# Optimization experiments

Hardware: AMD Instinct MI355X
Metric: run time of the kernel (lower is better)

Reference implementation:

```python
import jax, jax.numpy as jnp
import numpy as np

B, T, S, D = 4, 4, 128, 256  # batch, turns, seq_len, hidden_size
H = D  # GRU units == hidden_size


def setup_inputs() -> dict:
    key = jax.random.key(0)
    ks = jax.random.split(key, 8)
    sc = lambda *sh: float(np.sqrt(2.0 / sum(sh[:2]))) if len(sh) > 1 else 0.05
    return {
        "features": jax.random.normal(ks[0], (B, T, S, D), jnp.float32),
        "w1": jax.random.normal(ks[1], (D, D), jnp.float32) * sc(D, D),
        "w2": jax.random.normal(ks[2], (D, D), jnp.float32) * sc(D, D),
        "bias": jax.random.normal(ks[3], (D,), jnp.float32) * 0.05,
        "v3": jax.random.normal(ks[4], (D,), jnp.float32) * 0.05,
        "gru_kernel": jax.random.normal(ks[5], (2 * D, 3 * H), jnp.float32) * sc(2 * D, 3 * H),
        "gru_rec_kernel": jax.random.normal(ks[6], (H, 3 * H), jnp.float32) * sc(H, 3 * H),
        "gru_bias": jax.random.normal(ks[7], (2, 3 * H), jnp.float32) * 0.05,
    }


def _gru(x, kernel, rec_kernel, bias):
    # x: [N, S, 2D]; Keras GRU (reset_after=True, tanh/sigmoid), h0 = 0.
    b_in, b_rec = bias[0], bias[1]
    xp = x @ kernel + b_in               # [N, S, 3H] input projections
    xp_t = jnp.swapaxes(xp, 0, 1)        # [S, N, 3H]
    h0 = jnp.zeros((x.shape[0], H), x.dtype)

    def step(h, xt):
        rp = h @ rec_kernel + b_rec      # [N, 3H]
        xz, xr, xh = jnp.split(xt, 3, axis=-1)
        rz, rr, rh = jnp.split(rp, 3, axis=-1)
        z = jax.nn.sigmoid(xz + rz)
        r = jax.nn.sigmoid(xr + rr)
        hh = jnp.tanh(xh + r * rh)
        h_new = z * h + (1.0 - z) * hh
        return h_new, h_new

    _, ys = jax.lax.scan(step, h0, xp_t)  # ys: [S, N, H]
    return jnp.swapaxes(ys, 0, 1)         # [N, S, H]


def reference(features, w1, w2, bias, v3, gru_kernel, gru_rec_kernel, gru_bias):
    b, t, s, d = features.shape
    x = features.reshape(b * t, s, d)     # fold turns into batch (same per-utterance math)
    left = jnp.einsum('bsd,dt->bst', x, w1)
    right = jnp.einsum('bsd,dt->bst', x, w2)
    # additive (Bahdanau) scores: [N, s, s, d] intermediate
    temp = jnp.tanh(left[:, :, None, :] + right[:, None, :, :] + bias)
    score = jax.nn.softmax(jnp.einsum('bmnd,d->bmn', temp, v3), axis=-1)
    c = jnp.einsum('bmn,bnd->bmd', score, x)
    p = _gru(jnp.concatenate([x, c], axis=-1), gru_kernel, gru_rec_kernel, gru_bias)
    return p.reshape(b, t, s, H)
```

## Files before the change

### kernel.cpp

```cpp
#include <hip/hip_runtime.h>
#include <hip/hip_bf16.h>

typedef __attribute__((ext_vector_type(8))) short short8;
typedef __attribute__((ext_vector_type(4))) float floatx4;

#define NSEQ 16
#define SEQ 128
#define DIM 256
#define HID 256
#define K3H 768
#define K2D 512
#define LOG2E 1.442695041f
#define LOG2E2 2.885390082f
#define WS_STRIDE 772

__device__ __forceinline__ float frcp(float x) { return __builtin_amdgcn_rcpf(x); }
__device__ __forceinline__ unsigned short bf16bits(float v) {
    unsigned u = __builtin_bit_cast(unsigned, v);
    unsigned r = (u + 0x7FFFu + ((u >> 16) & 1u)) >> 16;
    return (unsigned short)r;
}
__device__ __forceinline__ void load_lds16(const float* gsrc, float* ldsbase) {
    __builtin_amdgcn_global_load_lds(
        (const __attribute__((address_space(1))) void*)gsrc,
        (__attribute__((address_space(3))) void*)ldsbase, 16, 0, 0);
}

__global__ __launch_bounds__(256) void k1_leftright(
        const float* __restrict__ x, const float* __restrict__ w1,
        const float* __restrict__ w2, float* __restrict__ left,
        float* __restrict__ right) {
    __shared__ __align__(16) float xs[8][DIM];
    const int tid = threadIdx.x;
    const int r0 = blockIdx.x * 8;
    #pragma unroll
    for (int i = 0; i < 8; ++i) xs[i][tid] = x[(r0 + i) * DIM + tid];
    __syncthreads();
    float accL[8], accR[8];
    #pragma unroll
    for (int i = 0; i < 8; ++i) { accL[i] = 0.f; accR[i] = 0.f; }
    #pragma unroll 4
    for (int d = 0; d < DIM; ++d) {
        float wa = w1[d * DIM + tid];
        float wb = w2[d * DIM + tid];
        #pragma unroll
        for (int i = 0; i < 8; ++i) {
            float xv = xs[i][d];
            accL[i] = fmaf(xv, wa, accL[i]);
            accR[i] = fmaf(xv, wb, accR[i]);
        }
    }
    #pragma unroll
    for (int i = 0; i < 8; ++i) {
        left[(r0 + i) * DIM + tid]  = accL[i] * LOG2E2;
        right[(r0 + i) * DIM + tid] = accR[i] * LOG2E2;
    }
}

__global__ __launch_bounds__(256) void k2_attn(
        const float* __restrict__ x, const float* __restrict__ left,
        const float* __restrict__ right, const float* __restrict__ bias,
        const float* __restrict__ v3, float* __restrict__ cout) {
    __shared__ __align__(16) float lm[4][DIM];
    __shared__ __align__(16) float v3s[DIM];
    __shared__ __align__(16) float P[4][SEQ];
    const int tid = threadIdx.x;
    const int b  = blockIdx.x >> 5;
    const int m0 = (blockIdx.x & 31) * 4;

    v3s[tid] = v3[tid];
    #pragma unroll
    for (int i = 0; i < 4; ++i)
        lm[i][tid] = left[(size_t)(b * SEQ + m0 + i) * DIM + tid] + bias[tid] * LOG2E2;
    __syncthreads();

    const int mi = tid >> 6;
    const int nl = tid & 63;
    float s0 = 0.f, s1 = 0.f;
    const float4* lv4 = reinterpret_cast<const float4*>(lm[mi]);
    const float4* vv4 = reinterpret_cast<const float4*>(v3s);
    const float4* r0v = reinterpret_cast<const float4*>(right + (size_t)(b * SEQ + nl) * DIM);
    const float4* r1v = reinterpret_cast<const float4*>(right + (size_t)(b * SEQ + nl + 64) * DIM);
    #pragma unroll 2
    for (int d4 = 0; d4 < DIM / 4; ++d4) {
        float4 lv = lv4[d4];
        float4 vv = vv4[d4];
        float4 ra = r0v[d4];
        float4 rb = r1v[d4];
        float a0 = 1.f - 2.f * frcp(1.f + __builtin_amdgcn_exp2f(lv.x + ra.x));
        float a1 = 1.f - 2.f * frcp(1.f + __builtin_amdgcn_exp2f(lv.y + ra.y));
        float a2 = 1.f - 2.f * frcp(1.f + __builtin_amdgcn_exp2f(lv.z + ra.z));
        float a3 = 1.f - 2.f * frcp(1.f + __builtin_amdgcn_exp2f(lv.w + ra.w));
        s0 = fmaf(a0, vv.x, s0); s0 = fmaf(a1, vv.y, s0);
        s0 = fmaf(a2, vv.z, s0); s0 = fmaf(a3, vv.w, s0);
        float b0 = 1.f - 2.f * frcp(1.f + __builtin_amdgcn_exp2f(lv.x + rb.x));
        float b1 = 1.f - 2.f * frcp(1.f + __builtin_amdgcn_exp2f(lv.y + rb.y));
        float b2 = 1.f - 2.f * frcp(1.f + __builtin_amdgcn_exp2f(lv.z + rb.z));
        float b3 = 1.f - 2.f * frcp(1.f + __builtin_amdgcn_exp2f(lv.w + rb.w));
        s1 = fmaf(b0, vv.x, s1); s1 = fmaf(b1, vv.y, s1);
        s1 = fmaf(b2, vv.z, s1); s1 = fmaf(b3, vv.w, s1);
    }
    float mx = fmaxf(s0, s1);
    #pragma unroll
    for (int off = 32; off >= 1; off >>= 1) mx = fmaxf(mx, __shfl_xor(mx, off, 64));
    float e0 = __expf(s0 - mx), e1 = __expf(s1 - mx);
    float sm = e0 + e1;
    #pragma unroll
    for (int off = 32; off >= 1; off >>= 1) sm += __shfl_xor(sm, off, 64);
    float inv = frcp(sm);
    P[mi][nl]      = e0 * inv;
    P[mi][nl + 64] = e1 * inv;
    __syncthreads();

    float acc[4] = {0.f, 0.f, 0.f, 0.f};
    const float* xb = x + (size_t)b * SEQ * DIM;
    for (int nc = 0; nc < SEQ / 4; ++nc) {
        float xv0 = xb[(nc * 4 + 0) * DIM + tid];
        float xv1 = xb[(nc * 4 + 1) * DIM + tid];
        float xv2 = xb[(nc * 4 + 2) * DIM + tid];
        float xv3 = xb[(nc * 4 + 3) * DIM + tid];
        #pragma unroll
        for (int i = 0; i < 4; ++i) {
            float4 pv = *reinterpret_cast<const float4*>(&P[i][nc * 4]);
            acc[i] = fmaf(pv.x, xv0, acc[i]);
            acc[i] = fmaf(pv.y, xv1, acc[i]);
            acc[i] = fmaf(pv.z, xv2, acc[i]);
            acc[i] = fmaf(pv.w, xv3, acc[i]);
        }
    }
    #pragma unroll
    for (int i = 0; i < 4; ++i)
        cout[(size_t)(b * SEQ + m0 + i) * DIM + tid] = acc[i];
}

__global__ __launch_bounds__(512) void k3_mfma(
        const float* __restrict__ x, const float* __restrict__ c,
        const float* __restrict__ gk, const float* __restrict__ gbias,
        float* __restrict__ xp) {
    __shared__ __align__(16) unsigned short As[64][72];
    __shared__ __align__(16) unsigned short Bs[192][72];
    const int tid  = threadIdx.x;
    const int lane = tid & 63;
    const int w    = tid >> 6;
    const int l15  = lane & 15;
    const int g4   = lane >> 4;
    const int wm   = w >> 2;
    const int wn   = w & 3;
    const int m0   = (blockIdx.x & 31) * 64;
    const int n0   = (blockIdx.x >> 5) * 192;

    floatx4 Cf[2][3];
    #pragma unroll
    for (int i = 0; i < 2; ++i)
        #pragma unroll
        for (int j = 0; j < 3; ++j) Cf[i][j] = (floatx4){0.f, 0.f, 0.f, 0.f};

    for (int ch = 0; ch < 8; ++ch) {
        const int kbase = ch * 64;
        #pragma unroll
        for (int q = 0; q < 2; ++q) {
            int fi = q * 512 + tid;
            int row = fi >> 4, kq = (fi & 15) << 2;
            int kg = kbase + kq;
            const float* src = (kg < 256) ? &x[(size_t)(m0 + row) * DIM + kg]
                                          : &c[(size_t)(m0 + row) * DIM + (kg - 256)];
            float4 v = *reinterpret_cast<const float4*>(src);
            unsigned short* dst = &As[row][kq];
            dst[0] = bf16bits(v.x); dst[1] = bf16bits(v.y);
            dst[2] = bf16bits(v.z); dst[3] = bf16bits(v.w);
        }
        #pragma unroll
        for (int q = 0; q < 6; ++q) {
            int fi = q * 512 + tid;
            int krow = fi / 48, nq = (fi % 48) << 2;
            float4 v = *reinterpret_cast<const float4*>(
                &gk[(size_t)(kbase + krow) * K3H + n0 + nq]);
            Bs[nq + 0][krow] = bf16bits(v.x);
            Bs[nq + 1][krow] = bf16bits(v.y);
            Bs[nq + 2][krow] = bf16bits(v.z);
            Bs[nq + 3][krow] = bf16bits(v.w);
        }
        __syncthreads();
        #pragma unroll
        for (int kk = 0; kk < 2; ++kk) {
            short8 af[2], bf[3];
            #pragma unroll
            for (int i = 0; i < 2; ++i)
                af[i] = *reinterpret_cast<const short8*>(&As[wm * 32 + i * 16 + l15][kk * 32 + g4 * 8]);
            #pragma unroll
            for (int j = 0; j < 3; ++j)
                bf[j] = *reinterpret_cast<const short8*>(&Bs[wn * 48 + j * 16 + l15][kk * 32 + g4 * 8]);
            #pragma unroll
            for (int i = 0; i < 2; ++i)
                #pragma unroll
                for (int j = 0; j < 3; ++j)
                    Cf[i][j] = __builtin_amdgcn_mfma_f32_16x16x32_bf16(af[i], bf[j], Cf[i][j], 0, 0, 0);
        }
        __syncthreads();
    }

    #pragma unroll
    for (int j = 0; j < 3; ++j) {
        const int nbase = n0 + wn * 48 + j * 16;
        const int col = nbase + l15;
        const float sc = (nbase >= 512) ? LOG2E2 : LOG2E;
        const float bv = ((col < 512) ? (gbias[col] + gbias[K3H + col]) : gbias[col]) * sc;
        #pragma unroll
        for (int i = 0; i < 2; ++i) {
            const int rbase = m0 + wm * 32 + i * 16 + g4 * 4;
            #pragma unroll
            for (int r = 0; r < 4; ++r)
                xp[(size_t)(rbase + r) * K3H + col] = fmaf(Cf[i][j][r], sc, bv);
        }
    }
}

__global__ __launch_bounds__(512) void k4_gru(
        const float* __restrict__ rec, const float* __restrict__ gbias,
        const float* __restrict__ xp, float* __restrict__ out) {
    __shared__ __align__(16) float ws[16 * WS_STRIDE];
    __shared__ __align__(16) float xq0[K3H], xq1[K3H], xq2[K3H];
    __shared__ __align__(16) unsigned short hbf[2][HID];
    const int tid  = threadIdx.x;
    const int lane = tid & 63;
    const int wv   = tid >> 6;
    const int seq  = blockIdx.x;
    const int l15  = lane & 15;
    const int g4   = lane >> 4;

    short8 Bf[6][8];
    #pragma unroll
    for (int part = 0; part < 16; ++part) {
        #pragma unroll
        for (int q = 0; q < 6; ++q) {
            int fi = q * 512 + tid;
            int row = fi / 192, c4 = fi % 192;
            reinterpret_cast<float4*>(ws)[row * (WS_STRIDE / 4) + c4] =
                reinterpret_cast<const float4*>(rec + part * 16 * K3H)[fi];
        }
        __syncthreads();
        const int kc = part >> 1, half = part & 1;
        #pragma unroll
        for (int u = 0; u < 6; ++u) {
            const float sc = (u >= 4) ? LOG2E2 : LOG2E;
            const int col = (u >> 1) * 256 + (u & 1) * 16 + wv * 32 + l15;
            #pragma unroll
            for (int j = 0; j < 8; ++j) {
                int r = g4 * 8 + j;
                if ((r >> 4) == half)
                    Bf[u][kc][j] = (short)bf16bits(ws[(r & 15) * WS_STRIDE + col] * sc);
            }
        }
        __syncthreads();
    }

    const int dd = wv * 32 + (lane & 31);
    const float brh_l = gbias[K3H + 512 + dd] * LOG2E2;
    const int tsel = (lane >> 4) & 1;

    const float* xps = xp + (size_t)seq * SEQ * K3H;
    float* outs = out + (size_t)seq * SEQ * HID;

    float h = 0.f;
    if (tid < HID) hbf[0][tid] = 0;

    if (wv < 3) {
        load_lds16(xps + wv * 256 + (lane << 2),       xq0 + wv * 256);
        load_lds16(xps + K3H + wv * 256 + (lane << 2), xq1 + wv * 256);
    }
    asm volatile("s_waitcnt vmcnt(0)" ::: "memory");
    __syncthreads();

    float* p0 = xq0;
    float* p1 = xq1;
    float* p2 = xq2;

    #define K4_STEP(s_, CB, NB)                                                         \
    {                                                                                   \
        const int sp = ((s_) + 2 < SEQ) ? (s_) + 2 : SEQ - 1;                           \
        if (wv < 3)                                                                     \
            load_lds16(xps + (size_t)sp * K3H + wv * 256 + (lane << 2), p2 + wv * 256); \
        short8 av[8];                                                                   \
        _Pragma("unroll")                                                               \
        for (int kc = 0; kc < 8; ++kc)                                                  \
            av[kc] = *reinterpret_cast<const short8*>(&hbf[CB][kc * 32 + g4 * 8]);      \
        const float xz = p0[dd];                                                        \
        const float xr = p0[256 + dd];                                                  \
        const float xh = p0[512 + dd];                                                  \
        floatx4 C[6];                                                                   \
        _Pragma("unroll")                                                               \
        for (int u = 0; u < 6; ++u) C[u] = (floatx4){0.f, 0.f, 0.f, 0.f};               \
        _Pragma("unroll")                                                               \
        for (int kc = 0; kc < 8; ++kc) {                                                \
            _Pragma("unroll")                                                           \
            for (int u = 0; u < 6; ++u)                                                 \
                C[u] = __builtin_amdgcn_mfma_f32_16x16x32_bf16(av[kc], Bf[u][kc],       \
                                                               C[u], 0, 0, 0);         \
        }                                                                               \
        if (lane < 32) {                                                                \
            float rz = tsel ? C[1][0] : C[0][0];                                        \
            float rr = tsel ? C[3][0] : C[2][0];                                        \
            float rh = tsel ? C[5][0] : C[4][0];                                        \
            float z  = frcp(1.f + __builtin_amdgcn_exp2f(-(rz + xz)));                  \
            float r  = frcp(1.f + __builtin_amdgcn_exp2f(-(rr + xr)));                  \
            float th = fmaf(r, rh + brh_l, xh);                                         \
            float hh = 1.f - 2.f * frcp(1.f + __builtin_amdgcn_exp2f(th));              \
            h = hh + z * (h - hh);                                                      \
            hbf[NB][dd] = bf16bits(h);                                                  \
            outs[(s_) * HID + dd] = h;                                                  \
        }                                                                               \
        asm volatile("s_waitcnt vmcnt(3) lgkmcnt(0)\n\ts_barrier" ::: "memory");        \
        float* tmp_ = p0; p0 = p1; p1 = p2; p2 = tmp_;                                  \
    }

    for (int s = 0; s < SEQ; s += 2) {
        K4_STEP(s,     0, 1)
        K4_STEP(s + 1, 1, 0)
    }
    #undef K4_STEP
}

extern "C" void kernel_launch(void* const* d_in, const int* in_sizes, int n_in,
                              void* d_out, int out_size, void* d_ws, size_t ws_size,
                              hipStream_t stream) {
    const float* feat = (const float*)d_in[0];
    const float* w1   = (const float*)d_in[1];
    const float* w2   = (const float*)d_in[2];
    const float* bias = (const float*)d_in[3];
    const float* v3   = (const float*)d_in[4];
    const float* gk   = (const float*)d_in[5];
    const float* grk  = (const float*)d_in[6];
    const float* gb   = (const float*)d_in[7];
    float* out = (float*)d_out;

    char* wsb = (char*)d_ws;
    float* left  = (float*)(wsb);
    float* right = (float*)(wsb + (size_t)2 * 1024 * 1024);
    float* cbuf  = (float*)(wsb + (size_t)4 * 1024 * 1024);
    float* xp    = (float*)(wsb + (size_t)6 * 1024 * 1024);

    k1_leftright<<<2048 / 8, 256, 0, stream>>>(feat, w1, w2, left, right);
    k2_attn<<<NSEQ * 32, 256, 0, stream>>>(feat, left, right, bias, v3, cbuf);
    k3_mfma<<<128, 512, 0, stream>>>(feat, cbuf, gk, gb, xp);
    k4_gru<<<NSEQ, 512, 0, stream>>>(grk, gb, xp, out);
}
```

Before: 238.0 us.

## Fuse all four stages into one persistent kernel with atomic-flag dataflow

Merges the four kernels (left/right projection, attention, input projection GEMM, GRU recurrence) into a single launch. Block ranges are assigned to stages, and global atomic counters act as dependency flags. The GRU blocks preload their recurrent weights into registers while upstream stages are still running, and start the recurrence once the first half of the input projections is ready. This is meant to remove launch gaps and overlap the serial GRU setup with producer work. The cost is spin-waiting on flags, a memset, and reliance on all 528 blocks being co-resident to avoid deadlock.

```diff
diff --git a/kernel.cpp b/kernel.cpp
--- a/kernel.cpp
+++ b/kernel.cpp
@@ -26,298 +26,339 @@
         (__attribute__((address_space(3))) void*)ldsbase, 16, 0, 0);
 }
 
-__global__ __launch_bounds__(256) void k1_leftright(
+__global__ __launch_bounds__(512) void k_fused(
         const float* __restrict__ x, const float* __restrict__ w1,
-        const float* __restrict__ w2, float* __restrict__ left,
-        float* __restrict__ right) {
-    __shared__ __align__(16) float xs[8][DIM];
+        const float* __restrict__ w2, const float* __restrict__ bias,
+        const float* __restrict__ v3, const float* __restrict__ gk,
+        const float* __restrict__ rec, const float* __restrict__ gb,
+        float* __restrict__ left, float* __restrict__ right,
+        float* __restrict__ cbuf, float* __restrict__ xp,
+        float* __restrict__ out, unsigned* __restrict__ flags) {
+    __shared__ __align__(16) char smem[59648];
+    unsigned* f1 = flags;
+    unsigned* f2 = flags + 16;
+    unsigned* f3 = flags + 48;
+    const int bid = blockIdx.x;
     const int tid = threadIdx.x;
-    const int r0 = blockIdx.x * 8;
-    #pragma unroll
-    for (int i = 0; i < 8; ++i) xs[i][tid] = x[(r0 + i) * DIM + tid];
-    __syncthreads();
-    float accL[8], accR[8];
-    #pragma unroll
-    for (int i = 0; i < 8; ++i) { accL[i] = 0.f; accR[i] = 0.f; }
-    #pragma unroll 4
-    for (int d = 0; d < DIM; ++d) {
-        float wa = w1[d * DIM + tid];
-        float wb = w2[d * DIM + tid];
+
+    if (bid < 16) {
+        float* ws = (float*)smem;
+        float* xqa = (float*)(smem + 49408);
+        float* xqb = (float*)(smem + 52480);
+        float* xqc = (float*)(smem + 55552);
+        unsigned short (*hbf)[HID] = (unsigned short(*)[HID])(smem + 58624);
+        const int lane = tid & 63;
+        const int wv   = tid >> 6;
+        const int seq  = bid;
+        const int l15  = lane & 15;
+        const int g4   = lane >> 4;
+
+        short8 Bf[6][8];
+        #pragma unroll
+        for (int part = 0; part < 16; ++part) {
+            #pragma unroll
+            for (int q = 0; q < 6; ++q) {
+                int fi = q * 512 + tid;
+                int row = fi / 192, c4 = fi % 192;
+                reinterpret_cast<float4*>(ws)[row * (WS_STRIDE / 4) + c4] =
+                    reinterpret_cast<const float4*>(rec + part * 16 * K3H)[fi];
+            }
+            __syncthreads();
+            const int kc = part >> 1, half = part & 1;
+            #pragma unroll
+            for (int u = 0; u < 6; ++u) {
+                const float sc = (u >= 4) ? LOG2E2 : LOG2E;
+                const int col = (u >> 1) * 256 + (u & 1) * 16 + wv * 32 + l15;
+                #pragma unroll
+                for (int j = 0; j < 8; ++j) {
+                    int r = g4 * 8 + j;
+                    if ((r >> 4) == half)
+                        Bf[u][kc][j] = (short)bf16bits(ws[(r & 15) * WS_STRIDE + col] * sc);
+                }
+            }
+            __syncthreads();
+        }
+
+        const int dd = wv * 32 + (lane & 31);
+        const float brh_l = gb[K3H + 512 + dd] * LOG2E2;
+        const int tsel = (lane >> 4) & 1;
+        const float* xps = xp + (size_t)seq * SEQ * K3H;
+        float* outs = out + (size_t)seq * SEQ * HID;
+        float h = 0.f;
+        if (tid < HID) hbf[0][tid] = 0;
+
+        if (tid == 0) { while (atomicAdd(&f3[seq * 2], 0u) < 4u) __builtin_amdgcn_s_sleep(2); }
+        __syncthreads();
+        __threadfence();
+
+        if (wv < 3) {
+            load_lds16(xps + wv * 256 + (lane << 2),       xqa + wv * 256);
+            load_lds16(xps + K3H + wv * 256 + (lane << 2), xqb + wv * 256);
+        }
+        asm volatile("s_waitcnt vmcnt(0)" ::: "memory");
+        __syncthreads();
+
+        float* p0 = xqa;
+        float* p1 = xqb;
+        float* p2 = xqc;
+
+        #define K4_STEP(s_, CB, NB)                                                         \
+        {                                                                                   \
+            const int sp = ((s_) + 2 < SEQ) ? (s_) + 2 : SEQ - 1;                           \
+            if (wv < 3)                                                                     \
+                load_lds16(xps + (size_t)sp * K3H + wv * 256 + (lane << 2), p2 + wv * 256); \
+            short8 av[8];                                                                   \
+            _Pragma("unroll")                                                               \
+            for (int kc = 0; kc < 8; ++kc)                                                  \
+                av[kc] = *reinterpret_cast<const short8*>(&hbf[CB][kc * 32 + g4 * 8]);      \
+            const float xz = p0[dd];                                                        \
+            const float xr = p0[256 + dd];                                                  \
+            const float xh = p0[512 + dd];                                                  \
+            floatx4 C[6];                                                                   \
+            _Pragma("unroll")                                                               \
+            for (int u = 0; u < 6; ++u) C[u] = (floatx4){0.f, 0.f, 0.f, 0.f};               \
+            _Pragma("unroll")                                                               \
+            for (int kc = 0; kc < 8; ++kc) {                                                \
+                _Pragma("unroll")                                                           \
+                for (int u = 0; u < 6; ++u)                                                 \
+                    C[u] = __builtin_amdgcn_mfma_f32_16x16x32_bf16(av[kc], Bf[u][kc],       \
+                                                                   C[u], 0, 0, 0);         \
+            }                                                                               \
+            if (lane < 32) {                                                                \
+                float rz = tsel ? C[1][0] : C[0][0];                                        \
+                float rr = tsel ? C[3][0] : C[2][0];                                        \
+                float rh = tsel ? C[5][0] : C[4][0];                                        \
+                float z  = frcp(1.f + __builtin_amdgcn_exp2f(-(rz + xz)));                  \
+                float r  = frcp(1.f + __builtin_amdgcn_exp2f(-(rr + xr)));                  \
+                float th = fmaf(r, rh + brh_l, xh);                                         \
+                float hh = 1.f - 2.f * frcp(1.f + __builtin_amdgcn_exp2f(th));              \
+                h = hh + z * (h - hh);                                                      \
+                hbf[NB][dd] = bf16bits(h);                                                  \
+                outs[(s_) * HID + dd] = h;                                                  \
+            }                                                                               \
+            asm volatile("s_waitcnt vmcnt(3) lgkmcnt(0)\n\ts_barrier" ::: "memory");        \
+            float* tmp_ = p0; p0 = p1; p1 = p2; p2 = tmp_;                                  \
+        }
+
+        for (int s = 0; s < 62; s += 2) {
+            K4_STEP(s,     0, 1)
+            K4_STEP(s + 1, 1, 0)
+        }
+        if (tid == 0) { while (atomicAdd(&f3[seq * 2 + 1], 0u) < 4u) __builtin_amdgcn_s_sleep(2); }
+        __syncthreads();
+        __threadfence();
+        for (int s = 62; s < SEQ; s += 2) {
+            K4_STEP(s,     0, 1)
+            K4_STEP(s + 1, 1, 0)
+        }
+        #undef K4_STEP
+
+    } else if (bid < 144) {
+        const int kb = bid - 16;
+        const int r0 = kb * 16;
+        float (*xs)[DIM] = (float(*)[DIM])smem;
+        const int col = tid & 255, hf = tid >> 8;
+        #pragma unroll
+        for (int i = 0; i < 8; ++i)
+            xs[hf * 8 + i][col] = x[(size_t)(r0 + hf * 8 + i) * DIM + col];
+        __syncthreads();
+        float accL[8], accR[8];
+        #pragma unroll
+        for (int i = 0; i < 8; ++i) { accL[i] = 0.f; accR[i] = 0.f; }
+        #pragma unroll 4
+        for (int d = 0; d < DIM; ++d) {
+            float wa = w1[d * DIM + col];
+            float wb = w2[d * DIM + col];
+            #pragma unroll
+            for (int i = 0; i < 8; ++i) {
+                float xv = xs[hf * 8 + i][d];
+                accL[i] = fmaf(xv, wa, accL[i]);
+                accR[i] = fmaf(xv, wb, accR[i]);
+            }
+        }
         #pragma unroll
         for (int i = 0; i < 8; ++i) {
-            float xv = xs[i][d];
-            accL[i] = fmaf(xv, wa, accL[i]);
-            accR[i] = fmaf(xv, wb, accR[i]);
-        }
+            left[(size_t)(r0 + hf * 8 + i) * DIM + col]  = accL[i] * LOG2E2;
+            right[(size_t)(r0 + hf * 8 + i) * DIM + col] = accR[i] * LOG2E2;
+        }
+        __threadfence();
+        __syncthreads();
+        if (tid == 0) atomicAdd(&f1[kb >> 3], 1u);
+
+    } else if (bid < 400) {
+        const int kb = bid - 144;
+        const int b  = kb >> 4;
+        const int m0 = (kb & 15) * 8;
+        float (*lm)[DIM] = (float(*)[DIM])smem;
+        float* v3s = (float*)(smem + 8192);
+        float (*P)[SEQ] = (float(*)[SEQ])(smem + 9216);
+
+        if (tid == 0) { while (atomicAdd(&f1[b], 0u) < 8u) __builtin_amdgcn_s_sleep(2); }
+        __syncthreads();
+        __threadfence();
+
+        {
+            const int col = tid & 255, hf = tid >> 8;
+            #pragma unroll
+            for (int i = 0; i < 4; ++i)
+                lm[hf * 4 + i][col] =
+                    left[(size_t)(b * SEQ + m0 + hf * 4 + i) * DIM + col] + bias[col] * LOG2E2;
+            if (tid < 256) v3s[tid] = v3[tid];
+        }
+        __syncthreads();
+
+        const int w  = tid >> 6;
+        const int nl = tid & 63;
+        float s0 = 0.f, s1 = 0.f;
+        const float4* lv4 = reinterpret_cast<const float4*>(lm[w]);
+        const float4* vv4 = reinterpret_cast<const float4*>(v3s);
+        const float4* r0v = reinterpret_cast<const float4*>(right + (size_t)(b * SEQ + nl) * DIM);
+        const float4* r1v = reinterpret_cast<const float4*>(right + (size_t)(b * SEQ + nl + 64) * DIM);
+        #pragma unroll 2
+        for (int d4 = 0; d4 < DIM / 4; ++d4) {
+            float4 lv = lv4[d4];
+            float4 vv = vv4[d4];
+            float4 ra = r0v[d4];
+            float4 rb = r1v[d4];
+            float a0 = 1.f - 2.f * frcp(1.f + __builtin_amdgcn_exp2f(lv.x + ra.x));
+            float a1 = 1.f - 2.f * frcp(1.f + __builtin_amdgcn_exp2f(lv.y + ra.y));
+            float a2 = 1.f - 2.f * frcp(1.f + __builtin_amdgcn_exp2f(lv.z + ra.z));
+            float a3 = 1.f - 2.f * frcp(1.f + __builtin_amdgcn_exp2f(lv.w + ra.w));
+            s0 = fmaf(a0, vv.x, s0); s0 = fmaf(a1, vv.y, s0);
+            s0 = fmaf(a2, vv.z, s0); s0 = fmaf(a3, vv.w, s0);
+            float b0 = 1.f - 2.f * frcp(1.f + __builtin_amdgcn_exp2f(lv.x + rb.x));
+            float b1 = 1.f - 2.f * frcp(1.f + __builtin_amdgcn_exp2f(lv.y + rb.y));
+            float b2 = 1.f - 2.f * frcp(1.f + __builtin_amdgcn_exp2f(lv.z + rb.z));
+            float b3 = 1.f - 2.f * frcp(1.f + __builtin_amdgcn_exp2f(lv.w + rb.w));
+            s1 = fmaf(b0, vv.x, s1); s1 = fmaf(b1, vv.y, s1);
+            s1 = fmaf(b2, vv.z, s1); s1 = fmaf(b3, vv.w, s1);
+        }
+        float mx = fmaxf(s0, s1);
+        #pragma unroll
+        for (int off = 32; off >= 1; off >>= 1) mx = fmaxf(mx, __shfl_xor(mx, off, 64));
+        float e0 = __expf(s0 - mx), e1 = __expf(s1 - mx);
+        float sm = e0 + e1;
+        #pragma unroll
+        for (int off = 32; off >= 1; off >>= 1) sm += __shfl_xor(sm, off, 64);
+        float inv = frcp(sm);
+        P[w][nl]      = e0 * inv;
+        P[w][nl + 64] = e1 * inv;
+        __syncthreads();
+
+        const int d  = tid & 255;
+        const int rg = tid >> 8;
+        float acc[4] = {0.f, 0.f, 0.f, 0.f};
+        const float* xb = x + (size_t)b * SEQ * DIM;
+        for (int nc = 0; nc < SEQ / 4; ++nc) {
+            float xv0 = xb[(nc * 4 + 0) * DIM + d];
+            float xv1 = xb[(nc * 4 + 1) * DIM + d];
+            float xv2 = xb[(nc * 4 + 2) * DIM + d];
+            float xv3 = xb[(nc * 4 + 3) * DIM + d];
+            #pragma unroll
+            for (int i = 0; i < 4; ++i) {
+                float4 pv = *reinterpret_cast<const float4*>(&P[rg * 4 + i][nc * 4]);
+                acc[i] = fmaf(pv.x, xv0, acc[i]);
+                acc[i] = fmaf(pv.y, xv1, acc[i]);
+                acc[i] = fmaf(pv.z, xv2, acc[i]);
+                acc[i] = fmaf(pv.w, xv3, acc[i]);
+            }
+        }
+        #pragma unroll
+        for (int i = 0; i < 4; ++i)
+            cbuf[(size_t)(b * SEQ + m0 + rg * 4 + i) * DIM + d] = acc[i];
+        __threadfence();
+        __syncthreads();
+        if (tid == 0) atomicAdd(&f2[b * 2 + (m0 >> 6)], 1u);
+
+    } else {
+        const int kb = bid - 400;
+        unsigned short (*As)[72] = (unsigned short(*)[72])smem;
+        unsigned short (*Bs)[72] = (unsigned short(*)[72])(smem + 9216);
+        const int lane = tid & 63;
+        const int w    = tid >> 6;
+        const int l15  = lane & 15;
+        const int g4   = lane >> 4;
+        const int wm   = w >> 2;
+        const int wn   = w & 3;
+        const int mt   = kb & 31;
+        const int m0   = mt * 64;
+        const int n0   = (kb >> 5) * 192;
+
+        if (tid == 0) {
+            while (atomicAdd(&f2[(m0 >> 7) * 2 + ((m0 >> 6) & 1)], 0u) < 8u)
+                __builtin_amdgcn_s_sleep(2);
+        }
+        __syncthreads();
+        __threadfence();
+
+        floatx4 Cf[2][3];
+        #pragma unroll
+        for (int i = 0; i < 2; ++i)
+            #pragma unroll
+            for (int j = 0; j < 3; ++j) Cf[i][j] = (floatx4){0.f, 0.f, 0.f, 0.f};
+
+        for (int ch = 0; ch < 8; ++ch) {
+            const int kbase = ch * 64;
+            #pragma unroll
+            for (int q = 0; q < 2; ++q) {
+                int fi = q * 512 + tid;
+                int row = fi >> 4, kq = (fi & 15) << 2;
+                int kg = kbase + kq;
+                const float* src = (kg < 256) ? &x[(size_t)(m0 + row) * DIM + kg]
+                                              : &cbuf[(size_t)(m0 + row) * DIM + (kg - 256)];
+                float4 v = *reinterpret_cast<const float4*>(src);
+                unsigned short* dst = &As[row][kq];
+                dst[0] = bf16bits(v.x); dst[1] = bf16bits(v.y);
+                dst[2] = bf16bits(v.z); dst[3] = bf16bits(v.w);
+            }
+            #pragma unroll
+            for (int q = 0; q < 6; ++q) {
+                int fi = q * 512 + tid;
+                int krow = fi / 48, nq = (fi % 48) << 2;
+                float4 v = *reinterpret_cast<const float4*>(
+                    &gk[(size_t)(kbase + krow) * K3H + n0 + nq]);
+                Bs[nq + 0][krow] = bf16bits(v.x);
+                Bs[nq + 1][krow] = bf16bits(v.y);
+                Bs[nq + 2][krow] = bf16bits(v.z);
+                Bs[nq + 3][krow] = bf16bits(v.w);
+            }
+            __syncthreads();
+            #pragma unroll
+            for (int kk = 0; kk < 2; ++kk) {
+                short8 af[2], bf[3];
+                #pragma unroll
+                for (int i = 0; i < 2; ++i)
+                    af[i] = *reinterpret_cast<const short8*>(&As[wm * 32 + i * 16 + l15][kk * 32 + g4 * 8]);
+                #pragma unroll
+                for (int j = 0; j < 3; ++j)
+                    bf[j] = *reinterpret_cast<const short8*>(&Bs[wn * 48 + j * 16 + l15][kk * 32 + g4 * 8]);
+                #pragma unroll
+                for (int i = 0; i < 2; ++i)
+                    #pragma unroll
+                    for (int j = 0; j < 3; ++j)
+                        Cf[i][j] = __builtin_amdgcn_mfma_f32_16x16x32_bf16(af[i], bf[j], Cf[i][j], 0, 0, 0);
+            }
+            __syncthreads();
+        }
+
+        #pragma unroll
+        for (int j = 0; j < 3; ++j) {
+            const int nbase = n0 + wn * 48 + j * 16;
+            const int col = nbase + l15;
+            const float sc = (nbase >= 512) ? LOG2E2 : LOG2E;
+            const float bv = ((col < 512) ? (gb[col] + gb[K3H + col]) : gb[col]) * sc;
+            #pragma unroll
+            for (int i = 0; i < 2; ++i) {
+                const int rbase = m0 + wm * 32 + i * 16 + g4 * 4;
+                #pragma unroll
+                for (int r = 0; r < 4; ++r)
+                    xp[(size_t)(rbase + r) * K3H + col] = fmaf(Cf[i][j][r], sc, bv);
+            }
+        }
+        __threadfence();
+        __syncthreads();
+        if (tid == 0) atomicAdd(&f3[mt], 1u);
     }
-    #pragma unroll
-    for (int i = 0; i < 8; ++i) {
-        left[(r0 + i) * DIM + tid]  = accL[i] * LOG2E2;
-        right[(r0 + i) * DIM + tid] = accR[i] * LOG2E2;
-    }
-}
-
-__global__ __launch_bounds__(256) void k2_attn(
-        const float* __restrict__ x, const float* __restrict__ left,
-        const float* __restrict__ right, const float* __restrict__ bias,
-        const float* __restrict__ v3, float* __restrict__ cout) {
-    __shared__ __align__(16) float lm[4][DIM];
-    __shared__ __align__(16) float v3s[DIM];
-    __shared__ __align__(16) float P[4][SEQ];
-    const int tid = threadIdx.x;
-    const int b  = blockIdx.x >> 5;
-    const int m0 = (blockIdx.x & 31) * 4;
-
-    v3s[tid] = v3[tid];
-    #pragma unroll
-    for (int i = 0; i < 4; ++i)
-        lm[i][tid] = left[(size_t)(b * SEQ + m0 + i) * DIM + tid] + bias[tid] * LOG2E2;
-    __syncthreads();
-
-    const int mi = tid >> 6;
-    const int nl = tid & 63;
-    float s0 = 0.f, s1 = 0.f;
-    const float4* lv4 = reinterpret_cast<const float4*>(lm[mi]);
-    const float4* vv4 = reinterpret_cast<const float4*>(v3s);
-    const float4* r0v = reinterpret_cast<const float4*>(right + (size_t)(b * SEQ + nl) * DIM);
-    const float4* r1v = reinterpret_cast<const float4*>(right + (size_t)(b * SEQ + nl + 64) * DIM);
-    #pragma unroll 2
-    for (int d4 = 0; d4 < DIM / 4; ++d4) {
-        float4 lv = lv4[d4];
-        float4 vv = vv4[d4];
-        float4 ra = r0v[d4];
-        float4 rb = r1v[d4];
-        float a0 = 1.f - 2.f * frcp(1.f + __builtin_amdgcn_exp2f(lv.x + ra.x));
-        float a1 = 1.f - 2.f * frcp(1.f + __builtin_amdgcn_exp2f(lv.y + ra.y));
-        float a2 = 1.f - 2.f * frcp(1.f + __builtin_amdgcn_exp2f(lv.z + ra.z));
-        float a3 = 1.f - 2.f * frcp(1.f + __builtin_amdgcn_exp2f(lv.w + ra.w));
-        s0 = fmaf(a0, vv.x, s0); s0 = fmaf(a1, vv.y, s0);
-        s0 = fmaf(a2, vv.z, s0); s0 = fmaf(a3, vv.w, s0);
-        float b0 = 1.f - 2.f * frcp(1.f + __builtin_amdgcn_exp2f(lv.x + rb.x));
-        float b1 = 1.f - 2.f * frcp(1.f + __builtin_amdgcn_exp2f(lv.y + rb.y));
-        float b2 = 1.f - 2.f * frcp(1.f + __builtin_amdgcn_exp2f(lv.z + rb.z));
-        float b3 = 1.f - 2.f * frcp(1.f + __builtin_amdgcn_exp2f(lv.w + rb.w));
-        s1 = fmaf(b0, vv.x, s1); s1 = fmaf(b1, vv.y, s1);
-        s1 = fmaf(b2, vv.z, s1); s1 = fmaf(b3, vv.w, s1);
-    }
-    float mx = fmaxf(s0, s1);
-    #pragma unroll
-    for (int off = 32; off >= 1; off >>= 1) mx = fmaxf(mx, __shfl_xor(mx, off, 64));
-    float e0 = __expf(s0 - mx), e1 = __expf(s1 - mx);
-    float sm = e0 + e1;
-    #pragma unroll
-    for (int off = 32; off >= 1; off >>= 1) sm += __shfl_xor(sm, off, 64);
-    float inv = frcp(sm);
-    P[mi][nl]      = e0 * inv;
-    P[mi][nl + 64] = e1 * inv;
-    __syncthreads();
-
-    float acc[4] = {0.f, 0.f, 0.f, 0.f};
-    const float* xb = x + (size_t)b * SEQ * DIM;
-    for (int nc = 0; nc < SEQ / 4; ++nc) {
-        float xv0 = xb[(nc * 4 + 0) * DIM + tid];
-        float xv1 = xb[(nc * 4 + 1) * DIM + tid];
-        float xv2 = xb[(nc * 4 + 2) * DIM + tid];
-        float xv3 = xb[(nc * 4 + 3) * DIM + tid];
-        #pragma unroll
-        for (int i = 0; i < 4; ++i) {
-            float4 pv = *reinterpret_cast<const float4*>(&P[i][nc * 4]);
-            acc[i] = fmaf(pv.x, xv0, acc[i]);
-            acc[i] = fmaf(pv.y, xv1, acc[i]);
-            acc[i] = fmaf(pv.z, xv2, acc[i]);
-            acc[i] = fmaf(pv.w, xv3, acc[i]);
-        }
-    }
-    #pragma unroll
-    for (int i = 0; i < 4; ++i)
-        cout[(size_t)(b * SEQ + m0 + i) * DIM + tid] = acc[i];
-}
-
-__global__ __launch_bounds__(512) void k3_mfma(
-        const float* __restrict__ x, const float* __restrict__ c,
-        const float* __restrict__ gk, const float* __restrict__ gbias,
-        float* __restrict__ xp) {
-    __shared__ __align__(16) unsigned short As[64][72];
-    __shared__ __align__(16) unsigned short Bs[192][72];
-    const int tid  = threadIdx.x;
-    const int lane = tid & 63;
-    const int w    = tid >> 6;
-    const int l15  = lane & 15;
-    const int g4   = lane >> 4;
-    const int wm   = w >> 2;
-    const int wn   = w & 3;
-    const int m0   = (blockIdx.x & 31) * 64;
-    const int n0   = (blockIdx.x >> 5) * 192;
-
-    floatx4 Cf[2][3];
-    #pragma unroll
-    for (int i = 0; i < 2; ++i)
-        #pragma unroll
-        for (int j = 0; j < 3; ++j) Cf[i][j] = (floatx4){0.f, 0.f, 0.f, 0.f};
-
-    for (int ch = 0; ch < 8; ++ch) {
-        const int kbase = ch * 64;
-        #pragma unroll
-        for (int q = 0; q < 2; ++q) {
-            int fi = q * 512 + tid;
-            int row = fi >> 4, kq = (fi & 15) << 2;
-            int kg = kbase + kq;
-            const float* src = (kg < 256) ? &x[(size_t)(m0 + row) * DIM + kg]
-                                          : &c[(size_t)(m0 + row) * DIM + (kg - 256)];
-            float4 v = *reinterpret_cast<const float4*>(src);
-            unsigned short* dst = &As[row][kq];
-            dst[0] = bf16bits(v.x); dst[1] = bf16bits(v.y);
-            dst[2] = bf16bits(v.z); dst[3] = bf16bits(v.w);
-        }
-        #pragma unroll
-        for (int q = 0; q < 6; ++q) {
-            int fi = q * 512 + tid;
-            int krow = fi / 48, nq = (fi % 48) << 2;
-            float4 v = *reinterpret_cast<const float4*>(
-                &gk[(size_t)(kbase + krow) * K3H + n0 + nq]);
-            Bs[nq + 0][krow] = bf16bits(v.x);
-            Bs[nq + 1][krow] = bf16bits(v.y);
-            Bs[nq + 2][krow] = bf16bits(v.z);
-            Bs[nq + 3][krow] = bf16bits(v.w);
-        }
-        __syncthreads();
-        #pragma unroll
-        for (int kk = 0; kk < 2; ++kk) {
-            short8 af[2], bf[3];
-            #pragma unroll
-            for (int i = 0; i < 2; ++i)
-                af[i] = *reinterpret_cast<const short8*>(&As[wm * 32 + i * 16 + l15][kk * 32 + g4 * 8]);
-            #pragma unroll
-            for (int j = 0; j < 3; ++j)
-                bf[j] = *reinterpret_cast<const short8*>(&Bs[wn * 48 + j * 16 + l15][kk * 32 + g4 * 8]);
-            #pragma unroll
-            for (int i = 0; i < 2; ++i)
-                #pragma unroll
-                for (int j = 0; j < 3; ++j)
-                    Cf[i][j] = __builtin_amdgcn_mfma_f32_16x16x32_bf16(af[i], bf[j], Cf[i][j], 0, 0, 0);
-        }
-        __syncthreads();
-    }
-
-    #pragma unroll
-    for (int j = 0; j < 3; ++j) {
-        const int nbase = n0 + wn * 48 + j * 16;
-        const int col = nbase + l15;
-        const float sc = (nbase >= 512) ? LOG2E2 : LOG2E;
-        const float bv = ((col < 512) ? (gbias[col] + gbias[K3H + col]) : gbias[col]) * sc;
-        #pragma unroll
-        for (int i = 0; i < 2; ++i) {
-            const int rbase = m0 + wm * 32 + i * 16 + g4 * 4;
-            #pragma unroll
-            for (int r = 0; r < 4; ++r)
-                xp[(size_t)(rbase + r) * K3H + col] = fmaf(Cf[i][j][r], sc, bv);
-        }
-    }
-}
-
-__global__ __launch_bounds__(512) void k4_gru(
-        const float* __restrict__ rec, const float* __restrict__ gbias,
-        const float* __restrict__ xp, float* __restrict__ out) {
-    __shared__ __align__(16) float ws[16 * WS_STRIDE];
-    __shared__ __align__(16) float xq0[K3H], xq1[K3H], xq2[K3H];
-    __shared__ __align__(16) unsigned short hbf[2][HID];
-    const int tid  = threadIdx.x;
-    const int lane = tid & 63;
-    const int wv   = tid >> 6;
-    const int seq  = blockIdx.x;
-    const int l15  = lane & 15;
-    const int g4   = lane >> 4;
-
-    short8 Bf[6][8];
-    #pragma unroll
-    for (int part = 0; part < 16; ++part) {
-        #pragma unroll
-        for (int q = 0; q < 6; ++q) {
-            int fi = q * 512 + tid;
-            int row = fi / 192, c4 = fi % 192;
-            reinterpret_cast<float4*>(ws)[row * (WS_STRIDE / 4) + c4] =
-                reinterpret_cast<const float4*>(rec + part * 16 * K3H)[fi];
-        }
-        __syncthreads();
-        const int kc = part >> 1, half = part & 1;
-        #pragma unroll
-        for (int u = 0; u < 6; ++u) {
-            const float sc = (u >= 4) ? LOG2E2 : LOG2E;
-            const int col = (u >> 1) * 256 + (u & 1) * 16 + wv * 32 + l15;
-            #pragma unroll
-            for (int j = 0; j < 8; ++j) {
-                int r = g4 * 8 + j;
-                if ((r >> 4) == half)
-                    Bf[u][kc][j] = (short)bf16bits(ws[(r & 15) * WS_STRIDE + col] * sc);
-            }
-        }
-        __syncthreads();
-    }
-
-    const int dd = wv * 32 + (lane & 31);
-    const float brh_l = gbias[K3H + 512 + dd] * LOG2E2;
-    const int tsel = (lane >> 4) & 1;
-
-    const float* xps = xp + (size_t)seq * SEQ * K3H;
-    float* outs = out + (size_t)seq * SEQ * HID;
-
-    float h = 0.f;
-    if (tid < HID) hbf[0][tid] = 0;
-
-    if (wv < 3) {
-        load_lds16(xps + wv * 256 + (lane << 2),       xq0 + wv * 256);
-        load_lds16(xps + K3H + wv * 256 + (lane << 2), xq1 + wv * 256);
-    }
-    asm volatile("s_waitcnt vmcnt(0)" ::: "memory");
-    __syncthreads();
-
-    float* p0 = xq0;
-    float* p1 = xq1;
-    float* p2 = xq2;
-
-    #define K4_STEP(s_, CB, NB)                                                         \
-    {                                                                                   \
-        const int sp = ((s_) + 2 < SEQ) ? (s_) + 2 : SEQ - 1;                           \
-        if (wv < 3)                                                                     \
-            load_lds16(xps + (size_t)sp * K3H + wv * 256 + (lane << 2), p2 + wv * 256); \
-        short8 av[8];                                                                   \
-        _Pragma("unroll")                                                               \
-        for (int kc = 0; kc < 8; ++kc)                                                  \
-            av[kc] = *reinterpret_cast<const short8*>(&hbf[CB][kc * 32 + g4 * 8]);      \
-        const float xz = p0[dd];                                                        \
-        const float xr = p0[256 + dd];                                                  \
-        const float xh = p0[512 + dd];                                                  \
-        floatx4 C[6];                                                                   \
-        _Pragma("unroll")                                                               \
-        for (int u = 0; u < 6; ++u) C[u] = (floatx4){0.f, 0.f, 0.f, 0.f};               \
-        _Pragma("unroll")                                                               \
-        for (int kc = 0; kc < 8; ++kc) {                                                \
-            _Pragma("unroll")                                                           \
-            for (int u = 0; u < 6; ++u)                                                 \
-                C[u] = __builtin_amdgcn_mfma_f32_16x16x32_bf16(av[kc], Bf[u][kc],       \
-                                                               C[u], 0, 0, 0);         \
-        }                                                                               \
-        if (lane < 32) {                                                                \
-            float rz = tsel ? C[1][0] : C[0][0];                                        \
-            float rr = tsel ? C[3][0] : C[2][0];                                        \
-            float rh = tsel ? C[5][0] : C[4][0];                                        \
-            float z  = frcp(1.f + __builtin_amdgcn_exp2f(-(rz + xz)));                  \
-            float r  = frcp(1.f + __builtin_amdgcn_exp2f(-(rr + xr)));                  \
-            float th = fmaf(r, rh + brh_l, xh);                                         \
-            float hh = 1.f - 2.f * frcp(1.f + __builtin_amdgcn_exp2f(th));              \
-            h = hh + z * (h - hh);                                                      \
-            hbf[NB][dd] = bf16bits(h);                                                  \
-            outs[(s_) * HID + dd] = h;                                                  \
-        }                                                                               \
-        asm volatile("s_waitcnt vmcnt(3) lgkmcnt(0)\n\ts_barrier" ::: "memory");        \
-        float* tmp_ = p0; p0 = p1; p1 = p2; p2 = tmp_;                                  \
-    }
-
-    for (int s = 0; s < SEQ; s += 2) {
-        K4_STEP(s,     0, 1)
-        K4_STEP(s + 1, 1, 0)
-    }
-    #undef K4_STEP
 }
 
 extern "C" void kernel_launch(void* const* d_in, const int* in_sizes, int n_in,
@@ -338,9 +379,9 @@
     float* right = (float*)(wsb + (size_t)2 * 1024 * 1024);
     float* cbuf  = (float*)(wsb + (size_t)4 * 1024 * 1024);
     float* xp    = (float*)(wsb + (size_t)6 * 1024 * 1024);
-
-    k1_leftright<<<2048 / 8, 256, 0, stream>>>(feat, w1, w2, left, right);
-    k2_attn<<<NSEQ * 32, 256, 0, stream>>>(feat, left, right, bias, v3, cbuf);
-    k3_mfma<<<128, 512, 0, stream>>>(feat, cbuf, gk, gb, xp);
-    k4_gru<<<NSEQ, 512, 0, stream>>>(grk, gb, xp, out);
+    unsigned* flags = (unsigned*)(wsb + (size_t)12 * 1024 * 1024);
+
+    hipMemsetAsync(flags, 0, 512, stream);
+    k_fused<<<528, 512, 0, stream>>>(feat, w1, w2, bias, v3, gk, grk, gb,
+                                     left, right, cbuf, xp, out, flags);
 }
```

Measured after the change: 397.2 us. 1.67x slower.
